# Performance work log

Hardware: AMD Instinct MI355X
Metric: run time of the kernel (lower is better)

## Reference

```python
import jax, jax.numpy as jnp
import numpy as np

B, S, HID, H = 1, 2048, 512, 8
D = HID // H            # head_dim = 64
N_TIP, N_FAC = 16, 256
SCALE = 1.0 / np.sqrt(D).astype(np.float32)


def _dominant_dim_indices():
    # dominant_fcs = arange(n_tip) % (head_dim//2), identical for every head
    pair_dim = max(1, D // 2)
    fc = jnp.arange(N_TIP) % pair_dim                      # [n_tip]
    dim_idx = jnp.stack((fc * 2, fc * 2 + 1), axis=-1).reshape(-1)  # [2*n_tip]
    return jnp.clip(dim_idx, 0, D - 1)


def setup_inputs() -> dict:
    key = jax.random.key(0)
    kx, kq, kk, kv, ko = jax.random.split(key, 5)
    s = 1.0 / np.sqrt(HID)
    return {
        "x": jax.random.normal(kx, (B, S, HID), jnp.float32),
        "wq": jax.random.normal(kq, (HID, HID), jnp.float32) * s,
        "wk": jax.random.normal(kk, (HID, HID), jnp.float32) * s,
        "wv": jax.random.normal(kv, (HID, HID), jnp.float32) * s,
        "wo": jax.random.normal(ko, (HID, HID), jnp.float32) * s,
    }


def reference(x, wq, wk, wv, wo):
    # projections (nn.Linear, no bias): y = x @ W.T; split into heads -> [B,H,S,D]
    def split_heads(y):
        return y.reshape(B, S, H, D).transpose(0, 2, 1, 3)

    q = split_heads(x @ wq.T)
    k = split_heads(x @ wk.T)
    v = split_heads(x @ wv.T)

    dim_idx = _dominant_dim_indices()                      # [2*n_tip]
    q_sub = q[..., dim_idx]                                # [B,H,S,2*n_tip]
    k_sub = k[..., dim_idx]
    importance = jnp.einsum("bhqf,bhkf->bhqk", q_sub, k_sub)  # [B,H,S,S]

    n_sel = min(N_FAC, S)
    _, top_idx = jax.lax.top_k(importance, n_sel)          # [B,H,S,n_sel]

    # gather selected K/V per query: [B,H,S,n_sel,D]
    k_sel = jnp.take_along_axis(k[:, :, None], top_idx[..., None], axis=3)
    v_sel = jnp.take_along_axis(v[:, :, None], top_idx[..., None], axis=3)

    scores = jnp.einsum("bhqd,bhqkd->bhqk", q, k_sel) * SCALE
    attn = jax.nn.softmax(scores, axis=-1)
    out = jnp.einsum("bhqk,bhqkd->bhqd", attn, v_sel)      # [B,H,S,D]

    out = out.transpose(0, 2, 1, 3).reshape(B, S, HID)
    return out @ wo.T
```

## Files before the change

kernel.cpp:

```cpp
#include <hip/hip_runtime.h>

#define S_LEN  2048
#define HIDDEN 512
#define NHEAD  8
#define DHEAD  64
#define NSEL   256
#define ROWS_A 8
#define SCALE_ 0.125f

#define WAVE_SYNC() __asm__ volatile("s_waitcnt lgkmcnt(0)" ::: "memory")

__device__ __forceinline__ unsigned mapu(float f) {
  unsigned u = __float_as_uint(f);
  return (u & 0x80000000u) ? ~u : (u | 0x80000000u);
}
__device__ __forceinline__ float unmapu(unsigned x) {
  return __uint_as_float((x & 0x80000000u) ? (x & 0x7FFFFFFFu) : ~x);
}

union H4 { _Float16 h[4]; uint2 u2; };

__device__ __forceinline__ void gemm_nt_body(const float* __restrict__ A,
                                             const float* __restrict__ B,
                                             float* __restrict__ C,
                                             int K, int N, int m0, int n0,
                                             float (*As)[68], float (*Bs)[68]) {
  const int t  = threadIdx.x;
  const int tx = t & 15, ty = t >> 4;
  const int rr = t >> 3, cc = (t & 7) << 2;
  float acc[4][4] = {};

  float4 fa0 = *(const float4*)&A[(size_t)(m0 + rr)      * K + cc];
  float4 fa1 = *(const float4*)&A[(size_t)(m0 + rr + 32) * K + cc];
  float4 fb0 = *(const float4*)&B[(size_t)(n0 + rr)      * K + cc];
  float4 fb1 = *(const float4*)&B[(size_t)(n0 + rr + 32) * K + cc];

  for (int k0 = 0; k0 < K; k0 += 32) {
    __syncthreads();
    As[cc + 0][rr] = fa0.x; As[cc + 1][rr] = fa0.y; As[cc + 2][rr] = fa0.z; As[cc + 3][rr] = fa0.w;
    As[cc + 0][rr + 32] = fa1.x; As[cc + 1][rr + 32] = fa1.y; As[cc + 2][rr + 32] = fa1.z; As[cc + 3][rr + 32] = fa1.w;
    Bs[cc + 0][rr] = fb0.x; Bs[cc + 1][rr] = fb0.y; Bs[cc + 2][rr] = fb0.z; Bs[cc + 3][rr] = fb0.w;
    Bs[cc + 0][rr + 32] = fb1.x; Bs[cc + 1][rr + 32] = fb1.y; Bs[cc + 2][rr + 32] = fb1.z; Bs[cc + 3][rr + 32] = fb1.w;
    __syncthreads();
    if (k0 + 32 < K) {
      fa0 = *(const float4*)&A[(size_t)(m0 + rr)      * K + k0 + 32 + cc];
      fa1 = *(const float4*)&A[(size_t)(m0 + rr + 32) * K + k0 + 32 + cc];
      fb0 = *(const float4*)&B[(size_t)(n0 + rr)      * K + k0 + 32 + cc];
      fb1 = *(const float4*)&B[(size_t)(n0 + rr + 32) * K + k0 + 32 + cc];
    }
#pragma unroll
    for (int kk = 0; kk < 32; ++kk) {
      const float4 a4 = *(const float4*)&As[kk][ty * 4];
      const float4 b4 = *(const float4*)&Bs[kk][tx * 4];
      const float a[4] = {a4.x, a4.y, a4.z, a4.w};
      const float b[4] = {b4.x, b4.y, b4.z, b4.w};
#pragma unroll
      for (int i = 0; i < 4; ++i)
#pragma unroll
        for (int j = 0; j < 4; ++j) acc[i][j] += a[i] * b[j];
    }
  }
#pragma unroll
  for (int i = 0; i < 4; ++i) {
    float4 o = make_float4(acc[i][0], acc[i][1], acc[i][2], acc[i][3]);
    *(float4*)&C[(size_t)(m0 + ty * 4 + i) * N + n0 + tx * 4] = o;
  }
}

__global__ __launch_bounds__(256) void gemm_nt(const float* __restrict__ A,
                                               const float* __restrict__ B,
                                               float* __restrict__ C,
                                               int M, int N, int K) {
  __shared__ float As[32][68];
  __shared__ float Bs[32][68];
  gemm_nt_body(A, B, C, K, N, blockIdx.x * 64, blockIdx.y * 64, As, Bs);
}

__global__ __launch_bounds__(256) void gemm_qkv(const float* __restrict__ x,
                                                const float* __restrict__ wq,
                                                const float* __restrict__ wk,
                                                const float* __restrict__ wv,
                                                float* __restrict__ Qb,
                                                float* __restrict__ Kb,
                                                float* __restrict__ Vb) {
  __shared__ float As[32][68];
  __shared__ float Bs[32][68];
  const int z = blockIdx.z;
  const float* B = (z == 0) ? wq : (z == 1) ? wk : wv;
  float*       C = (z == 0) ? Qb : (z == 1) ? Kb : Vb;
  gemm_nt_body(x, B, C, HIDDEN, HIDDEN, blockIdx.x * 64, blockIdx.y * 64, As, Bs);
}

__global__ __launch_bounds__(256) void score_gemm(const float* __restrict__ Q,
                                                  const float* __restrict__ K,
                                                  unsigned* __restrict__ impu,
                                                  _Float16* __restrict__ sch) {
  __shared__ float Qs[64][132];
  __shared__ float Ks[64][68];
  const int bid  = blockIdx.x;
  const int h    = bid & (NHEAD - 1);
  const int tile = bid >> 3;
  const int q0   = (tile & 15) * 128;
  const int k0   = (tile >> 4) * 64;
  const int t  = threadIdx.x;
  const int tx = t & 15, ty = t >> 4;

#pragma unroll
  for (int s = 0; s < 8; ++s) {
    const int sf = s * 256 + t;
    const int r = sf >> 4, c = (sf & 15) * 4;
    const float4 f = *(const float4*)&Q[(size_t)(q0 + r) * HIDDEN + h * DHEAD + c];
    Qs[c + 0][r] = f.x; Qs[c + 1][r] = f.y; Qs[c + 2][r] = f.z; Qs[c + 3][r] = f.w;
  }
#pragma unroll
  for (int s = 0; s < 4; ++s) {
    const int sf = s * 256 + t;
    const int r = sf >> 4, c = (sf & 15) * 4;
    const float4 f = *(const float4*)&K[(size_t)(k0 + r) * HIDDEN + h * DHEAD + c];
    Ks[c + 0][r] = f.x; Ks[c + 1][r] = f.y; Ks[c + 2][r] = f.z; Ks[c + 3][r] = f.w;
  }
  __syncthreads();

  float acc[8][4] = {};
#pragma unroll
  for (int d = 0; d < 32; ++d) {
    const float4 aa = *(const float4*)&Qs[d][ty * 8];
    const float4 ab = *(const float4*)&Qs[d][ty * 8 + 4];
    const float4 b4 = *(const float4*)&Ks[d][tx * 4];
    const float a[8] = {aa.x, aa.y, aa.z, aa.w, ab.x, ab.y, ab.z, ab.w};
    const float b[4] = {b4.x, b4.y, b4.z, b4.w};
#pragma unroll
    for (int i = 0; i < 8; ++i)
#pragma unroll
      for (int j = 0; j < 4; ++j) acc[i][j] += a[i] * b[j];
  }
  float simp[8][4];
#pragma unroll
  for (int i = 0; i < 8; ++i)
#pragma unroll
    for (int j = 0; j < 4; ++j) simp[i][j] = acc[i][j];
#pragma unroll
  for (int d = 32; d < 64; ++d) {
    const float4 aa = *(const float4*)&Qs[d][ty * 8];
    const float4 ab = *(const float4*)&Qs[d][ty * 8 + 4];
    const float4 b4 = *(const float4*)&Ks[d][tx * 4];
    const float a[8] = {aa.x, aa.y, aa.z, aa.w, ab.x, ab.y, ab.z, ab.w};
    const float b[4] = {b4.x, b4.y, b4.z, b4.w};
#pragma unroll
    for (int i = 0; i < 8; ++i)
#pragma unroll
      for (int j = 0; j < 4; ++j) acc[i][j] += a[i] * b[j];
  }

#pragma unroll
  for (int i = 0; i < 8; ++i) {
    const size_t gr = (size_t)(h * S_LEN) + q0 + ty * 8 + i;
    const size_t off = gr * S_LEN + k0 + tx * 4;
    *(uint4*)&impu[off] = make_uint4(mapu(simp[i][0]), mapu(simp[i][1]),
                                     mapu(simp[i][2]), mapu(simp[i][3]));
    H4 pk;
#pragma unroll
    for (int j = 0; j < 4; ++j) pk.h[j] = (_Float16)(acc[i][j] * SCALE_);
    *(uint2*)&sch[off] = pk.u2;
  }
}

__global__ __launch_bounds__(512) void fused_select_pv(const unsigned* __restrict__ impu,
                                                       const _Float16* __restrict__ sch,
                                                       const float* __restrict__ V,
                                                       float* __restrict__ AO) {
  __shared__ unsigned hist[ROWS_A][256];
  __shared__ float    sbuf[ROWS_A][NSEL];
  __shared__ unsigned ibuf[ROWS_A][NSEL];
  __shared__ unsigned short eqbuf[ROWS_A][64];
  __shared__ unsigned rstate[ROWS_A][2];

  const int t = threadIdx.x, wv = t >> 6, lane = t & 63;
  const unsigned long long lmask = (1ull << lane) - 1ull;
  const size_t gr = (size_t)blockIdx.x * ROWS_A + wv;
  const unsigned* rowp  = impu + gr * S_LEN;
  const _Float16* shrow = sch  + gr * S_LEN;

  uint4 u[8];
  H4    s4[8];
#pragma unroll
  for (int j = 0; j < 8; ++j) {
    u[j]     = *(const uint4*)&rowp[j * 256 + lane * 4];
    s4[j].u2 = *(const uint2*)&shrow[j * 256 + lane * 4];
  }

  unsigned um = u[0].x, uM = u[0].x;
#pragma unroll
  for (int j = 0; j < 8; ++j) {
    um = min(um, min(min(u[j].x, u[j].y), min(u[j].z, u[j].w)));
    uM = max(uM, max(max(u[j].x, u[j].y), max(u[j].z, u[j].w)));
  }
#pragma unroll
  for (int off = 32; off; off >>= 1) {
    um = min(um, (unsigned)__shfl_xor((int)um, off));
    uM = max(uM, (unsigned)__shfl_xor((int)uM, off));
  }

  unsigned bn[8];
  unsigned T;
  if (uM == um) {
    T = uM;
  } else {
    const float vmin  = unmapu(um);
    const float scale = 255.0f / (unmapu(uM) - vmin);

    *(uint4*)&hist[wv][lane * 4] = make_uint4(0u, 0u, 0u, 0u);
    WAVE_SYNC();
#pragma unroll
    for (int j = 0; j < 8; ++j) {
      const unsigned uu[4] = {u[j].x, u[j].y, u[j].z, u[j].w};
      unsigned pk = 0;
#pragma unroll
      for (int e = 0; e < 4; ++e) {
        int bb = (int)((unmapu(uu[e]) - vmin) * scale);
        bb = bb < 0 ? 0 : (bb > 255 ? 255 : bb);
        pk |= (unsigned)bb << (8 * e);
        atomicAdd(&hist[wv][bb], 1u);
      }
      bn[j] = pk;
    }
    WAVE_SYNC();
    {
      const int g = 63 - lane;
      const uint4 c4 = *(const uint4*)&hist[wv][4 * g];
      const unsigned c0 = c4.x, c1 = c4.y, c2 = c4.z, c3 = c4.w;
      const unsigned lsum = c0 + c1 + c2 + c3;
      unsigned incl = lsum;
#pragma unroll
      for (int off = 1; off < 64; off <<= 1) {
        unsigned o = __shfl_up(incl, off);
        if (lane >= off) incl += o;
      }
      const unsigned excl = incl - lsum;
      const unsigned ab3 = excl, ab2 = excl + c3, ab1 = excl + c3 + c2, ab0 = excl + c3 + c2 + c1;
      if (ab3 < NSEL && NSEL <= ab3 + c3) { rstate[wv][0] = 4u*g+3u; rstate[wv][1] = NSEL - ab3; }
      if (ab2 < NSEL && NSEL <= ab2 + c2) { rstate[wv][0] = 4u*g+2u; rstate[wv][1] = NSEL - ab2; }
      if (ab1 < NSEL && NSEL <= ab1 + c1) { rstate[wv][0] = 4u*g+1u; rstate[wv][1] = NSEL - ab1; }
      if (ab0 < NSEL && NSEL <= ab0 + c0) { rstate[wv][0] = 4u*g+0u; rstate[wv][1] = NSEL - ab0; }
    }
    WAVE_SYNC();
    const unsigned B    = rstate[wv][0];
    const unsigned krem = rstate[wv][1];
    const unsigned nb   = hist[wv][B];

    if (nb <= 64) {
      unsigned* ebufu = (unsigned*)&sbuf[wv][0];
      unsigned nbase = 0;
#pragma unroll
      for (int j = 0; j < 8; ++j) {
        const unsigned uu[4] = {u[j].x, u[j].y, u[j].z, u[j].w};
#pragma unroll
        for (int e = 0; e < 4; ++e) {
          const bool inb = (((bn[j] >> (8 * e)) & 0xFFu) == B);
          const unsigned long long m = __ballot(inb);
          if (inb) ebufu[nbase + (unsigned)__popcll(m & lmask)] = uu[e];
          nbase += (unsigned)__popcll(m);
        }
      }
      WAVE_SYNC();
      const unsigned myv = (lane < (int)nb) ? ebufu[lane] : 0u;
      unsigned gtc = 0, eqc = 0;
      for (unsigned jj = 0; jj < nb; ++jj) {
        const unsigned bv = (unsigned)__shfl((int)myv, (int)jj);
        gtc += (bv > myv) ? 1u : 0u;
        eqc += (bv == myv) ? 1u : 0u;
      }
      if (lane < (int)nb && gtc < krem && krem <= gtc + eqc) rstate[wv][0] = myv;
      WAVE_SYNC();
      T = rstate[wv][0];
    } else {
      unsigned m2min = 0xFFFFFFFFu, m2max = 0u;
      for (int i = lane; i < S_LEN; i += 64) {
        const unsigned x = rowp[i];
        int bb = (int)((unmapu(x) - vmin) * scale);
        bb = bb < 0 ? 0 : (bb > 255 ? 255 : bb);
        if (bb == (int)B) { m2min = min(m2min, x); m2max = max(m2max, x); }
      }
#pragma unroll
      for (int off = 32; off; off >>= 1) {
        m2min = min(m2min, (unsigned)__shfl_xor((int)m2min, off));
        m2max = max(m2max, (unsigned)__shfl_xor((int)m2max, off));
      }
      if (m2max == m2min) {
        T = m2max;
      } else {
        const float vlo2   = unmapu(m2min);
        const float scale2 = 255.0f / (unmapu(m2max) - vlo2);
        *(uint4*)&hist[wv][lane * 4] = make_uint4(0u, 0u, 0u, 0u);
        WAVE_SYNC();
        for (int i = lane; i < S_LEN; i += 64) {
          const unsigned x = rowp[i];
          const float v = unmapu(x);
          int bb = (int)((v - vmin) * scale);
          bb = bb < 0 ? 0 : (bb > 255 ? 255 : bb);
          if (bb == (int)B) {
            int b2 = (int)((v - vlo2) * scale2);
            b2 = b2 < 0 ? 0 : (b2 > 255 ? 255 : b2);
            atomicAdd(&hist[wv][b2], 1u);
          }
        }
        WAVE_SYNC();
        {
          const int g = 63 - lane;
          const uint4 c4 = *(const uint4*)&hist[wv][4 * g];
          const unsigned c0 = c4.x, c1 = c4.y, c2 = c4.z, c3 = c4.w;
          const unsigned lsum = c0 + c1 + c2 + c3;
          unsigned incl = lsum;
#pragma unroll
          for (int off = 1; off < 64; off <<= 1) {
            unsigned o = __shfl_up(incl, off);
            if (lane >= off) incl += o;
          }
          const unsigned excl = incl - lsum;
          const unsigned ab3 = excl, ab2 = excl + c3, ab1 = excl + c3 + c2, ab0 = excl + c3 + c2 + c1;
          if (ab3 < krem && krem <= ab3 + c3) { rstate[wv][0] = 4u*g+3u; rstate[wv][1] = krem - ab3; }
          if (ab2 < krem && krem <= ab2 + c2) { rstate[wv][0] = 4u*g+2u; rstate[wv][1] = krem - ab2; }
          if (ab1 < krem && krem <= ab1 + c1) { rstate[wv][0] = 4u*g+1u; rstate[wv][1] = krem - ab1; }
          if (ab0 < krem && krem <= ab0 + c0) { rstate[wv][0] = 4u*g+0u; rstate[wv][1] = krem - ab0; }
        }
        WAVE_SYNC();
        const unsigned B2    = rstate[wv][0];
        const unsigned krem2 = rstate[wv][1];
        const unsigned nb2   = hist[wv][B2];
        if (nb2 <= 64) {
          unsigned* ebufu = (unsigned*)&sbuf[wv][0];
          unsigned nbase = 0;
          for (int i = lane; i < S_LEN; i += 64) {
            const unsigned x = rowp[i];
            const float v = unmapu(x);
            int bb = (int)((v - vmin) * scale);
            bb = bb < 0 ? 0 : (bb > 255 ? 255 : bb);
            bool inb = false;
            if (bb == (int)B) {
              int b2 = (int)((v - vlo2) * scale2);
              b2 = b2 < 0 ? 0 : (b2 > 255 ? 255 : b2);
              inb = (b2 == (int)B2);
            }
            const unsigned long long m = __ballot(inb);
            if (inb) ebufu[nbase + (unsigned)__popcll(m & lmask)] = x;
            nbase += (unsigned)__popcll(m);
          }
          WAVE_SYNC();
          const unsigned myv = (lane < (int)nb2) ? ebufu[lane] : 0u;
          unsigned gtc = 0, eqc = 0;
          for (unsigned jj = 0; jj < nb2; ++jj) {
            const unsigned bv = (unsigned)__shfl((int)myv, (int)jj);
            gtc += (bv > myv) ? 1u : 0u;
            eqc += (bv == myv) ? 1u : 0u;
          }
          if (lane < (int)nb2 && gtc < krem2 && krem2 <= gtc + eqc) rstate[wv][0] = myv;
          WAVE_SYNC();
          T = rstate[wv][0];
        } else {
          if (lane == 0) {
            unsigned pfx = 0, kr = NSEL;
            for (int rb = 3; rb >= 0; --rb) {
              for (int i2 = 0; i2 < 256; ++i2) hist[wv][i2] = 0u;
              for (int i2 = 0; i2 < S_LEN; ++i2) {
                const unsigned x = rowp[i2];
                if (rb == 3 || ((x >> (rb * 8 + 8)) == pfx)) hist[wv][(x >> (rb * 8)) & 0xFF]++;
              }
              unsigned cum = 0, sel = 0;
              for (int bb2 = 255; bb2 >= 0; --bb2) {
                if (kr <= cum + hist[wv][bb2]) { sel = (unsigned)bb2; kr -= cum; break; }
                cum += hist[wv][bb2];
              }
              pfx = (pfx << 8) | sel;
            }
            rstate[wv][0] = pfx;
          }
          WAVE_SYNC();
          T = rstate[wv][0];
        }
      }
    }
  }

  unsigned base_gt = 0, base_eq = 0;
#pragma unroll
  for (int j = 0; j < 8; ++j) {
    const unsigned uu[4] = {u[j].x, u[j].y, u[j].z, u[j].w};
#pragma unroll
    for (int e = 0; e < 4; ++e) {
      const unsigned v = uu[e];
      const int i = j * 256 + lane * 4 + e;
      const bool gt = (v > T), eq = (v == T);
      const unsigned long long mg = __ballot(gt);
      const unsigned long long me = __ballot(eq);
      if (gt) {
        const unsigned p = base_gt + (unsigned)__popcll(mg & lmask);
        ibuf[wv][p] = (unsigned)i << 9;
        sbuf[wv][p] = (float)s4[j].h[e];
      }
      if (eq) {
        const unsigned p = base_eq + (unsigned)__popcll(me & lmask);
        if (p < 64) eqbuf[wv][p] = (unsigned short)i;
      }
      base_gt += (unsigned)__popcll(mg);
      base_eq += (unsigned)__popcll(me);
    }
  }
  WAVE_SYNC();
  const unsigned ngt = base_gt, ne = base_eq;
  const unsigned need = NSEL - ngt;
  if (ne == need && ne <= 64) {
    for (unsigned j = lane; j < ne; j += 64) {
      const unsigned short ix = eqbuf[wv][j];
      ibuf[wv][ngt + j] = (unsigned)ix << 9;
      sbuf[wv][ngt + j] = (float)shrow[ix];
    }
  } else if (lane == 0) {
    if (ne <= 64) {
      for (unsigned j = 0; j < need; ++j) {
        const unsigned short ix = eqbuf[wv][j];
        ibuf[wv][ngt + j] = (unsigned)ix << 9;
        sbuf[wv][ngt + j] = (float)shrow[ix];
      }
    } else {
      unsigned taken = 0;
      for (int i = 0; i < S_LEN && taken < need; ++i)
        if (rowp[i] == T) { ibuf[wv][ngt + taken] = (unsigned)i << 9; sbuf[wv][ngt + taken] = (float)shrow[i]; ++taken; }
    }
  }
  WAVE_SYNC();

  float sc[4];
#pragma unroll
  for (int m = 0; m < 4; ++m) sc[m] = sbuf[wv][lane * 4 + m];
  float mx = fmaxf(fmaxf(sc[0], sc[1]), fmaxf(sc[2], sc[3]));
#pragma unroll
  for (int off = 32; off; off >>= 1) mx = fmaxf(mx, __shfl_xor(mx, off));
  float zs = 0.f;
#pragma unroll
  for (int m = 0; m < 4; ++m) { sc[m] = expf(sc[m] - mx); zs += sc[m]; }
#pragma unroll
  for (int off = 32; off; off >>= 1) zs += __shfl_xor(zs, off);
  const float rz = 1.0f / zs;
  *(float4*)&sbuf[wv][lane * 4] = make_float4(sc[0], sc[1], sc[2], sc[3]);
  WAVE_SYNC();

  const int h = (int)(gr >> 11), q = (int)(gr & (S_LEN - 1));
  const float* Vhl = V + h * DHEAD + lane;
  float outv = 0.f;
#pragma unroll 8
  for (int j = 0; j < NSEL; j += 4) {
    const uint4  id4 = *(const uint4*)&ibuf[wv][j];
    const float4 w4  = *(const float4*)&sbuf[wv][j];
    outv += w4.x * Vhl[id4.x];
    outv += w4.y * Vhl[id4.y];
    outv += w4.z * Vhl[id4.z];
    outv += w4.w * Vhl[id4.w];
  }
  AO[(size_t)q * HIDDEN + h * DHEAD + lane] = outv * rz;
}

__global__ __launch_bounds__(256) void imp_gemm(const float* __restrict__ Q,
                                                const float* __restrict__ K,
                                                unsigned* __restrict__ impu) {
  __shared__ float Qs[32][68];
  __shared__ float Ks[32][68];
  const int bid  = blockIdx.x;
  const int h    = bid & (NHEAD - 1);
  const int tile = bid >> 3;
  const int q0   = (tile & 31) * 64;
  const int k0   = (tile >> 5) * 64;
  const int t  = threadIdx.x;
  const int tx = t & 15, ty = t >> 4;
#pragma unroll
  for (int s = 0; s < 2; ++s) {
    int slot = t + s * 256;
    int r = slot >> 3, c = (slot & 7) << 2;
    const float4 fq = *(const float4*)&Q[(size_t)(q0 + r) * HIDDEN + h * DHEAD + c];
    Qs[c + 0][r] = fq.x; Qs[c + 1][r] = fq.y; Qs[c + 2][r] = fq.z; Qs[c + 3][r] = fq.w;
    const float4 fk = *(const float4*)&K[(size_t)(k0 + r) * HIDDEN + h * DHEAD + c];
    Ks[c + 0][r] = fk.x; Ks[c + 1][r] = fk.y; Ks[c + 2][r] = fk.z; Ks[c + 3][r] = fk.w;
  }
  __syncthreads();
  float acc[4][4] = {};
#pragma unroll
  for (int d = 0; d < 32; ++d) {
    const float4 a4 = *(const float4*)&Qs[d][ty * 4];
    const float4 b4 = *(const float4*)&Ks[d][tx * 4];
    const float a[4] = {a4.x, a4.y, a4.z, a4.w};
    const float b[4] = {b4.x, b4.y, b4.z, b4.w};
#pragma unroll
    for (int i = 0; i < 4; ++i)
#pragma unroll
      for (int j = 0; j < 4; ++j) acc[i][j] += a[i] * b[j];
  }
#pragma unroll
  for (int i = 0; i < 4; ++i) {
    uint4 o = make_uint4(mapu(acc[i][0]), mapu(acc[i][1]), mapu(acc[i][2]), mapu(acc[i][3]));
    *(uint4*)&impu[((size_t)(h * S_LEN) + q0 + ty * 4 + i) * S_LEN + k0 + tx * 4] = o;
  }
}

__global__ __launch_bounds__(512) void radix_select(const unsigned* __restrict__ impu,
                                                    unsigned short* __restrict__ selg) {
  __shared__ unsigned hist[ROWS_A][256];
  __shared__ unsigned short selbuf[ROWS_A][NSEL];
  __shared__ unsigned short eqbuf[ROWS_A][64];
  __shared__ unsigned cnt[ROWS_A], eqcnt[ROWS_A];
  __shared__ unsigned rstate[ROWS_A][2];

  const int t = threadIdx.x, wv = t >> 6, lane = t & 63;
  const size_t gr = (size_t)blockIdx.x * ROWS_A + wv;
  const unsigned* rowp = impu + gr * S_LEN;

  uint4 u[8];
#pragma unroll
  for (int j = 0; j < 8; ++j) u[j] = *(const uint4*)&rowp[j * 256 + lane * 4];

  unsigned prefix = 0, krem = NSEL;
#pragma unroll 1
  for (int b = 3; b >= 0; --b) {
    hist[wv][lane] = 0; hist[wv][lane + 64] = 0; hist[wv][lane + 128] = 0; hist[wv][lane + 192] = 0;
    WAVE_SYNC();
    const int shift = b * 8;
#pragma unroll
    for (int j = 0; j < 8; ++j) {
      const unsigned uu[4] = {u[j].x, u[j].y, u[j].z, u[j].w};
#pragma unroll
      for (int e = 0; e < 4; ++e) {
        const unsigned v = uu[e];
        const bool ok = (b == 3) || ((v >> (shift + 8)) == prefix);
        if (ok) atomicAdd(&hist[wv][(v >> shift) & 0xFF], 1u);
      }
    }
    WAVE_SYNC();
    const int g = 63 - lane;
    const uint4 c4 = *(const uint4*)&hist[wv][4 * g];
    const unsigned c0 = c4.x, c1 = c4.y, c2 = c4.z, c3 = c4.w;
    const unsigned lsum = c0 + c1 + c2 + c3;
    unsigned incl = lsum;
#pragma unroll
    for (int off = 1; off < 64; off <<= 1) {
      unsigned o = __shfl_up(incl, off);
      if (lane >= off) incl += o;
    }
    const unsigned excl = incl - lsum;
    const unsigned ab3 = excl, ab2 = excl + c3, ab1 = excl + c3 + c2, ab0 = excl + c3 + c2 + c1;
    if (ab3 < krem && krem <= ab3 + c3) { rstate[wv][0] = 4u*g+3u; rstate[wv][1] = krem - ab3; }
    if (ab2 < krem && krem <= ab2 + c2) { rstate[wv][0] = 4u*g+2u; rstate[wv][1] = krem - ab2; }
    if (ab1 < krem && krem <= ab1 + c1) { rstate[wv][0] = 4u*g+1u; rstate[wv][1] = krem - ab1; }
    if (ab0 < krem && krem <= ab0 + c0) { rstate[wv][0] = 4u*g+0u; rstate[wv][1] = krem - ab0; }
    WAVE_SYNC();
    prefix = (prefix << 8) | rstate[wv][0];
    krem   = rstate[wv][1];
  }
  const unsigned T = prefix;

  if (lane == 0) { cnt[wv] = 0; eqcnt[wv] = 0; }
  WAVE_SYNC();
#pragma unroll
  for (int j = 0; j < 8; ++j) {
    const unsigned uu[4] = {u[j].x, u[j].y, u[j].z, u[j].w};
#pragma unroll
    for (int e = 0; e < 4; ++e) {
      const unsigned v = uu[e];
      const int i = j * 256 + lane * 4 + e;
      if (v > T)       { unsigned p = atomicAdd(&cnt[wv], 1u);   selbuf[wv][p] = (unsigned short)i; }
      else if (v == T) { unsigned p = atomicAdd(&eqcnt[wv], 1u); if (p < 64) eqbuf[wv][p] = (unsigned short)i; }
    }
  }
  WAVE_SYNC();
  const unsigned ngt = cnt[wv], ne = eqcnt[wv];
  const unsigned need = NSEL - ngt;
  if (ne == need && ne <= 64) {
    for (unsigned j = lane; j < ne; j += 64) selbuf[wv][ngt + j] = eqbuf[wv][j];
  } else if (lane == 0) {
    if (ne <= 64) {
      for (unsigned a = 1; a < ne; ++a) {
        unsigned short kv = eqbuf[wv][a]; int bp = (int)a;
        while (bp > 0 && eqbuf[wv][bp - 1] > kv) { eqbuf[wv][bp] = eqbuf[wv][bp - 1]; --bp; }
        eqbuf[wv][bp] = kv;
      }
      for (unsigned j = 0; j < need; ++j) selbuf[wv][ngt + j] = eqbuf[wv][j];
    } else {
      unsigned taken = 0;
      for (int i = 0; i < S_LEN && taken < need; ++i)
        if (rowp[i] == T) { selbuf[wv][ngt + taken] = (unsigned short)i; ++taken; }
    }
  }
  WAVE_SYNC();
  if (lane < 32) {
    const uint4 o = *(const uint4*)&selbuf[wv][lane * 8];
    *(uint4*)&selg[gr * NSEL + lane * 8] = o;
  }
}

__global__ __launch_bounds__(256, 4) void fasa_attend(const float* __restrict__ Q,
                                                      const float* __restrict__ K,
                                                      const float* __restrict__ V,
                                                      const unsigned short* __restrict__ selg,
                                                      float* __restrict__ O) {
  __shared__ float qs[4][DHEAD];
  __shared__ float wbuf[4][NSEL];
  __shared__ int   ibuf[4][NSEL];
  const int bid = blockIdx.x;
  const int h   = bid & (NHEAD - 1);
  const int qb  = bid >> 3;
  const int t   = threadIdx.x, wv = t >> 6, lane = t & 63;
  const int row = qb * 4 + wv;

  qs[wv][lane] = Q[(size_t)row * HIDDEN + h * DHEAD + lane];
  const unsigned short* srow = selg + ((size_t)(h * S_LEN) + row) * NSEL;
  const ushort4 s4 = *(const ushort4*)&srow[lane * 4];
  int sidx[4] = {(int)s4.x, (int)s4.y, (int)s4.z, (int)s4.w};
  WAVE_SYNC();

  const float* Kh = K + h * DHEAD;
  float sc[4] = {0.f, 0.f, 0.f, 0.f};
#pragma unroll
  for (int k4 = 0; k4 < 16; ++k4) {
    const float4 qv = *(const float4*)&qs[wv][k4 * 4];
#pragma unroll
    for (int m = 0; m < 4; ++m) {
      const float4 kf = *(const float4*)&Kh[(size_t)sidx[m] * HIDDEN + k4 * 4];
      sc[m] += kf.x * qv.x + kf.y * qv.y + kf.z * qv.z + kf.w * qv.w;
    }
  }
#pragma unroll
  for (int m = 0; m < 4; ++m) sc[m] *= SCALE_;

  float mx = fmaxf(fmaxf(sc[0], sc[1]), fmaxf(sc[2], sc[3]));
#pragma unroll
  for (int off = 32; off; off >>= 1) mx = fmaxf(mx, __shfl_xor(mx, off));
  float zs = 0.f;
#pragma unroll
  for (int m = 0; m < 4; ++m) { sc[m] = expf(sc[m] - mx); zs += sc[m]; }
#pragma unroll
  for (int off = 32; off; off >>= 1) zs += __shfl_xor(zs, off);
  const float rz = 1.0f / zs;

  *(float4*)&wbuf[wv][lane * 4] = make_float4(sc[0], sc[1], sc[2], sc[3]);
  *(int4*)&ibuf[wv][lane * 4]   = make_int4(sidx[0], sidx[1], sidx[2], sidx[3]);
  WAVE_SYNC();

  const float* Vh = V + h * DHEAD;
  float outv = 0.f;
#pragma unroll 4
  for (int j = 0; j < NSEL; j += 4) {
    const int4   id4 = *(const int4*)&ibuf[wv][j];
    const float4 w4  = *(const float4*)&wbuf[wv][j];
    outv += w4.x * Vh[(size_t)id4.x * HIDDEN + lane];
    outv += w4.y * Vh[(size_t)id4.y * HIDDEN + lane];
    outv += w4.z * Vh[(size_t)id4.z * HIDDEN + lane];
    outv += w4.w * Vh[(size_t)id4.w * HIDDEN + lane];
  }
  O[(size_t)row * HIDDEN + h * DHEAD + lane] = outv * rz;
}

extern "C" void kernel_launch(void* const* d_in, const int* in_sizes, int n_in,
                              void* d_out, int out_size, void* d_ws, size_t ws_size,
                              hipStream_t stream) {
  const float* x  = (const float*)d_in[0];
  const float* wq = (const float*)d_in[1];
  const float* wk = (const float*)d_in[2];
  const float* wv = (const float*)d_in[3];
  const float* wo = (const float*)d_in[4];
  float* out = (float*)d_out;

  float* Qb = (float*)d_ws;
  float* Kb = Qb + (size_t)S_LEN * HIDDEN;
  float* Vb = Kb + (size_t)S_LEN * HIDDEN;
  float* AO = Vb + (size_t)S_LEN * HIDDEN;
  void*  tail = (void*)(AO + (size_t)S_LEN * HIDDEN);

  const size_t elems = (size_t)NHEAD * S_LEN * S_LEN;
  const size_t base  = (size_t)4 * S_LEN * HIDDEN * 4;
  const size_t need_new = base + elems * 4 + elems * 2;

  dim3 g(S_LEN / 64, HIDDEN / 64);
  gemm_qkv<<<dim3(S_LEN / 64, HIDDEN / 64, 3), 256, 0, stream>>>(x, wq, wk, wv, Qb, Kb, Vb);
  if (ws_size >= need_new) {
    unsigned* impu = (unsigned*)tail;
    _Float16* sch  = (_Float16*)(impu + elems);
    score_gemm<<<dim3(NHEAD * 16 * 32), 256, 0, stream>>>(Qb, Kb, impu, sch);
    fused_select_pv<<<dim3(NHEAD * S_LEN / ROWS_A), 512, 0, stream>>>(impu, sch, Vb, AO);
  } else {
    unsigned short* selg = (unsigned short*)tail;
    unsigned* impu = (unsigned*)(selg + (size_t)NHEAD * S_LEN * NSEL);
    imp_gemm<<<dim3(NHEAD * 32 * 32), 256, 0, stream>>>(Qb, Kb, impu);
    radix_select<<<dim3(NHEAD * S_LEN / ROWS_A), 512, 0, stream>>>(impu, selg);
    fasa_attend<<<dim3((S_LEN / 4) * NHEAD), 256, 0, stream>>>(Qb, Kb, Vb, selg, AO);
  }
  gemm_nt<<<g, 256, 0, stream>>>(AO, wo, out, S_LEN, HIDDEN, HIDDEN);
}
```

Measured before the change: 224.7 us.

## Fuse score GEMM with top-k select and PV into one LDS-resident kernel

Merges the score GEMM and the select/softmax/PV kernel into a single kernel. Each 512-thread block computes the importance and score rows for 8 queries of one head directly into LDS, then runs the radix select from LDS, which removes the large global writes and reads of the full S×S importance and score matrices. The cost is low arithmetic reuse, since every block streams all of K for its head and reads Q rows straight from global memory inside the inner loop. The heavy LDS use (about 136 KB per block) also limits occupancy, and a tie-sorting step is added to the serial fallback path.

New measurement: 519.9 us. 2.31x slower.

```diff
diff --git a/kernel.cpp b/kernel.cpp
--- a/kernel.cpp
+++ b/kernel.cpp
@@ -5,7 +5,7 @@
 #define NHEAD  8
 #define DHEAD  64
 #define NSEL   256
-#define ROWS_A 8
+#define ROWS_M 8
 #define SCALE_ 0.125f
 
 #define WAVE_SYNC() __asm__ volatile("s_waitcnt lgkmcnt(0)" ::: "memory")
@@ -91,95 +91,91 @@
   gemm_nt_body(x, B, C, HIDDEN, HIDDEN, blockIdx.x * 64, blockIdx.y * 64, As, Bs);
 }
 
-__global__ __launch_bounds__(256) void score_gemm(const float* __restrict__ Q,
-                                                  const float* __restrict__ K,
-                                                  unsigned* __restrict__ impu,
-                                                  _Float16* __restrict__ sch) {
-  __shared__ float Qs[64][132];
-  __shared__ float Ks[64][68];
-  const int bid  = blockIdx.x;
-  const int h    = bid & (NHEAD - 1);
-  const int tile = bid >> 3;
-  const int q0   = (tile & 15) * 128;
-  const int k0   = (tile >> 4) * 64;
-  const int t  = threadIdx.x;
-  const int tx = t & 15, ty = t >> 4;
-
-#pragma unroll
-  for (int s = 0; s < 8; ++s) {
-    const int sf = s * 256 + t;
-    const int r = sf >> 4, c = (sf & 15) * 4;
-    const float4 f = *(const float4*)&Q[(size_t)(q0 + r) * HIDDEN + h * DHEAD + c];
-    Qs[c + 0][r] = f.x; Qs[c + 1][r] = f.y; Qs[c + 2][r] = f.z; Qs[c + 3][r] = f.w;
-  }
-#pragma unroll
-  for (int s = 0; s < 4; ++s) {
-    const int sf = s * 256 + t;
-    const int r = sf >> 4, c = (sf & 15) * 4;
-    const float4 f = *(const float4*)&K[(size_t)(k0 + r) * HIDDEN + h * DHEAD + c];
-    Ks[c + 0][r] = f.x; Ks[c + 1][r] = f.y; Ks[c + 2][r] = f.z; Ks[c + 3][r] = f.w;
+__global__ __launch_bounds__(512) void mega_attn(const float* __restrict__ Qb,
+                                                 const float* __restrict__ Kb,
+                                                 const float* __restrict__ Vb,
+                                                 float* __restrict__ AO) {
+  __shared__ unsigned impL[ROWS_M][S_LEN];
+  __shared__ _Float16 scoreL[ROWS_M][S_LEN];
+  __shared__ __align__(16) char upool[40960];
+
+  float (*Kt)[20]            = (float (*)[20])upool;
+  unsigned (*hist)[256]      = (unsigned (*)[256])upool;
+  float (*sbuf)[256]         = (float (*)[256])(upool + 8192);
+  unsigned (*ibuf)[256]      = (unsigned (*)[256])(upool + 16384);
+  unsigned short (*eqbuf)[64]= (unsigned short (*)[64])(upool + 24576);
+  unsigned (*rstate)[2]      = (unsigned (*)[2])(upool + 25600);
+
+  const int bid = blockIdx.x;
+  const int h   = bid & (NHEAD - 1);
+  const int qb  = bid >> 3;
+  const int t   = threadIdx.x;
+  const int wv  = t >> 6, lane = t & 63;
+
+  {
+    float acc[ROWS_M], simp[ROWS_M];
+#pragma unroll
+    for (int r = 0; r < ROWS_M; ++r) acc[r] = 0.f;
+
+    float4 pf[4];
+#pragma unroll
+    for (int i = 0; i < 4; ++i) {
+      const int s = t + 512 * i;
+      const int key = s >> 2, part = (s & 3) * 4;
+      pf[i] = *(const float4*)&Kb[(size_t)key * HIDDEN + h * DHEAD + part];
+    }
+
+#pragma unroll 1
+    for (int cc = 0; cc < 16; ++cc) {
+      const int ks = cc >> 2, dc = cc & 3;
+      __syncthreads();
+#pragma unroll
+      for (int i = 0; i < 4; ++i) {
+        const int s = t + 512 * i;
+        *(float4*)&Kt[s >> 2][(s & 3) * 4] = pf[i];
+      }
+      __syncthreads();
+      if (cc < 15) {
+        const int nks = (cc + 1) >> 2, ndc = (cc + 1) & 3;
+#pragma unroll
+        for (int i = 0; i < 4; ++i) {
+          const int s = t + 512 * i;
+          const int key = s >> 2, part = (s & 3) * 4;
+          pf[i] = *(const float4*)&Kb[(size_t)(nks * 512 + key) * HIDDEN + h * DHEAD + ndc * 16 + part];
+        }
+      }
+      const float4 ka = *(const float4*)&Kt[t][0];
+      const float4 kb = *(const float4*)&Kt[t][4];
+      const float4 kc = *(const float4*)&Kt[t][8];
+      const float4 kd = *(const float4*)&Kt[t][12];
+      const float kk[16] = {ka.x, ka.y, ka.z, ka.w, kb.x, kb.y, kb.z, kb.w,
+                            kc.x, kc.y, kc.z, kc.w, kd.x, kd.y, kd.z, kd.w};
+#pragma unroll
+      for (int r = 0; r < ROWS_M; ++r) {
+        const float* qp = &Qb[(size_t)(qb * ROWS_M + r) * HIDDEN + h * DHEAD + dc * 16];
+#pragma unroll
+        for (int dd = 0; dd < 16; ++dd) acc[r] += kk[dd] * qp[dd];
+      }
+      if (dc == 1) {
+#pragma unroll
+        for (int r = 0; r < ROWS_M; ++r) simp[r] = acc[r];
+      }
+      if (dc == 3) {
+#pragma unroll
+        for (int r = 0; r < ROWS_M; ++r) {
+          impL[r][ks * 512 + t]   = mapu(simp[r]);
+          scoreL[r][ks * 512 + t] = (_Float16)(acc[r] * SCALE_);
+        }
+#pragma unroll
+        for (int r = 0; r < ROWS_M; ++r) acc[r] = 0.f;
+      }
+    }
   }
   __syncthreads();
 
-  float acc[8][4] = {};
-#pragma unroll
-  for (int d = 0; d < 32; ++d) {
-    const float4 aa = *(const float4*)&Qs[d][ty * 8];
-    const float4 ab = *(const float4*)&Qs[d][ty * 8 + 4];
-    const float4 b4 = *(const float4*)&Ks[d][tx * 4];
-    const float a[8] = {aa.x, aa.y, aa.z, aa.w, ab.x, ab.y, ab.z, ab.w};
-    const float b[4] = {b4.x, b4.y, b4.z, b4.w};
-#pragma unroll
-    for (int i = 0; i < 8; ++i)
-#pragma unroll
-      for (int j = 0; j < 4; ++j) acc[i][j] += a[i] * b[j];
-  }
-  float simp[8][4];
-#pragma unroll
-  for (int i = 0; i < 8; ++i)
-#pragma unroll
-    for (int j = 0; j < 4; ++j) simp[i][j] = acc[i][j];
-#pragma unroll
-  for (int d = 32; d < 64; ++d) {
-    const float4 aa = *(const float4*)&Qs[d][ty * 8];
-    const float4 ab = *(const float4*)&Qs[d][ty * 8 + 4];
-    const float4 b4 = *(const float4*)&Ks[d][tx * 4];
-    const float a[8] = {aa.x, aa.y, aa.z, aa.w, ab.x, ab.y, ab.z, ab.w};
-    const float b[4] = {b4.x, b4.y, b4.z, b4.w};
-#pragma unroll
-    for (int i = 0; i < 8; ++i)
-#pragma unroll
-      for (int j = 0; j < 4; ++j) acc[i][j] += a[i] * b[j];
-  }
-
-#pragma unroll
-  for (int i = 0; i < 8; ++i) {
-    const size_t gr = (size_t)(h * S_LEN) + q0 + ty * 8 + i;
-    const size_t off = gr * S_LEN + k0 + tx * 4;
-    *(uint4*)&impu[off] = make_uint4(mapu(simp[i][0]), mapu(simp[i][1]),
-                                     mapu(simp[i][2]), mapu(simp[i][3]));
-    H4 pk;
-#pragma unroll
-    for (int j = 0; j < 4; ++j) pk.h[j] = (_Float16)(acc[i][j] * SCALE_);
-    *(uint2*)&sch[off] = pk.u2;
-  }
-}
-
-__global__ __launch_bounds__(512) void fused_select_pv(const unsigned* __restrict__ impu,
-                                                       const _Float16* __restrict__ sch,
-                                                       const float* __restrict__ V,
-                                                       float* __restrict__ AO) {
-  __shared__ unsigned hist[ROWS_A][256];
-  __shared__ float    sbuf[ROWS_A][NSEL];
-  __shared__ unsigned ibuf[ROWS_A][NSEL];
-  __shared__ unsigned short eqbuf[ROWS_A][64];
-  __shared__ unsigned rstate[ROWS_A][2];
-
-  const int t = threadIdx.x, wv = t >> 6, lane = t & 63;
   const unsigned long long lmask = (1ull << lane) - 1ull;
-  const size_t gr = (size_t)blockIdx.x * ROWS_A + wv;
-  const unsigned* rowp  = impu + gr * S_LEN;
-  const _Float16* shrow = sch  + gr * S_LEN;
+  const unsigned* rowp  = &impL[wv][0];
+  const _Float16* shrow = &scoreL[wv][0];
 
   uint4 u[8];
   H4    s4[8];
@@ -416,6 +412,11 @@
     }
   } else if (lane == 0) {
     if (ne <= 64) {
+      for (unsigned a = 1; a < ne; ++a) {
+        unsigned short kv = eqbuf[wv][a]; int bp = (int)a;
+        while (bp > 0 && eqbuf[wv][bp - 1] > kv) { eqbuf[wv][bp] = eqbuf[wv][bp - 1]; --bp; }
+        eqbuf[wv][bp] = kv;
+      }
       for (unsigned j = 0; j < need; ++j) {
         const unsigned short ix = eqbuf[wv][j];
         ibuf[wv][ngt + j] = (unsigned)ix << 9;
@@ -444,8 +445,8 @@
   *(float4*)&sbuf[wv][lane * 4] = make_float4(sc[0], sc[1], sc[2], sc[3]);
   WAVE_SYNC();
 
-  const int h = (int)(gr >> 11), q = (int)(gr & (S_LEN - 1));
-  const float* Vhl = V + h * DHEAD + lane;
+  const int q = qb * ROWS_M + wv;
+  const float* Vhl = Vb + h * DHEAD + lane;
   float outv = 0.f;
 #pragma unroll 8
   for (int j = 0; j < NSEL; j += 4) {
@@ -459,203 +460,6 @@
   AO[(size_t)q * HIDDEN + h * DHEAD + lane] = outv * rz;
 }
 
-__global__ __launch_bounds__(256) void imp_gemm(const float* __restrict__ Q,
-                                                const float* __restrict__ K,
-                                                unsigned* __restrict__ impu) {
-  __shared__ float Qs[32][68];
-  __shared__ float Ks[32][68];
-  const int bid  = blockIdx.x;
-  const int h    = bid & (NHEAD - 1);
-  const int tile = bid >> 3;
-  const int q0   = (tile & 31) * 64;
-  const int k0   = (tile >> 5) * 64;
-  const int t  = threadIdx.x;
-  const int tx = t & 15, ty = t >> 4;
-#pragma unroll
-  for (int s = 0; s < 2; ++s) {
-    int slot = t + s * 256;
-    int r = slot >> 3, c = (slot & 7) << 2;
-    const float4 fq = *(const float4*)&Q[(size_t)(q0 + r) * HIDDEN + h * DHEAD + c];
-    Qs[c + 0][r] = fq.x; Qs[c + 1][r] = fq.y; Qs[c + 2][r] = fq.z; Qs[c + 3][r] = fq.w;
-    const float4 fk = *(const float4*)&K[(size_t)(k0 + r) * HIDDEN + h * DHEAD + c];
-    Ks[c + 0][r] = fk.x; Ks[c + 1][r] = fk.y; Ks[c + 2][r] = fk.z; Ks[c + 3][r] = fk.w;
-  }
-  __syncthreads();
-  float acc[4][4] = {};
-#pragma unroll
-  for (int d = 0; d < 32; ++d) {
-    const float4 a4 = *(const float4*)&Qs[d][ty * 4];
-    const float4 b4 = *(const float4*)&Ks[d][tx * 4];
-    const float a[4] = {a4.x, a4.y, a4.z, a4.w};
-    const float b[4] = {b4.x, b4.y, b4.z, b4.w};
-#pragma unroll
-    for (int i = 0; i < 4; ++i)
-#pragma unroll
-      for (int j = 0; j < 4; ++j) acc[i][j] += a[i] * b[j];
-  }
-#pragma unroll
-  for (int i = 0; i < 4; ++i) {
-    uint4 o = make_uint4(mapu(acc[i][0]), mapu(acc[i][1]), mapu(acc[i][2]), mapu(acc[i][3]));
-    *(uint4*)&impu[((size_t)(h * S_LEN) + q0 + ty * 4 + i) * S_LEN + k0 + tx * 4] = o;
-  }
-}
-
-__global__ __launch_bounds__(512) void radix_select(const unsigned* __restrict__ impu,
-                                                    unsigned short* __restrict__ selg) {
-  __shared__ unsigned hist[ROWS_A][256];
-  __shared__ unsigned short selbuf[ROWS_A][NSEL];
-  __shared__ unsigned short eqbuf[ROWS_A][64];
-  __shared__ unsigned cnt[ROWS_A], eqcnt[ROWS_A];
-  __shared__ unsigned rstate[ROWS_A][2];
-
-  const int t = threadIdx.x, wv = t >> 6, lane = t & 63;
-  const size_t gr = (size_t)blockIdx.x * ROWS_A + wv;
-  const unsigned* rowp = impu + gr * S_LEN;
-
-  uint4 u[8];
-#pragma unroll
-  for (int j = 0; j < 8; ++j) u[j] = *(const uint4*)&rowp[j * 256 + lane * 4];
-
-  unsigned prefix = 0, krem = NSEL;
-#pragma unroll 1
-  for (int b = 3; b >= 0; --b) {
-    hist[wv][lane] = 0; hist[wv][lane + 64] = 0; hist[wv][lane + 128] = 0; hist[wv][lane + 192] = 0;
-    WAVE_SYNC();
-    const int shift = b * 8;
-#pragma unroll
-    for (int j = 0; j < 8; ++j) {
-      const unsigned uu[4] = {u[j].x, u[j].y, u[j].z, u[j].w};
-#pragma unroll
-      for (int e = 0; e < 4; ++e) {
-        const unsigned v = uu[e];
-        const bool ok = (b == 3) || ((v >> (shift + 8)) == prefix);
-        if (ok) atomicAdd(&hist[wv][(v >> shift) & 0xFF], 1u);
-      }
-    }
-    WAVE_SYNC();
-    const int g = 63 - lane;
-    const uint4 c4 = *(const uint4*)&hist[wv][4 * g];
-    const unsigned c0 = c4.x, c1 = c4.y, c2 = c4.z, c3 = c4.w;
-    const unsigned lsum = c0 + c1 + c2 + c3;
-    unsigned incl = lsum;
-#pragma unroll
-    for (int off = 1; off < 64; off <<= 1) {
-      unsigned o = __shfl_up(incl, off);
-      if (lane >= off) incl += o;
-    }
-    const unsigned excl = incl - lsum;
-    const unsigned ab3 = excl, ab2 = excl + c3, ab1 = excl + c3 + c2, ab0 = excl + c3 + c2 + c1;
-    if (ab3 < krem && krem <= ab3 + c3) { rstate[wv][0] = 4u*g+3u; rstate[wv][1] = krem - ab3; }
-    if (ab2 < krem && krem <= ab2 + c2) { rstate[wv][0] = 4u*g+2u; rstate[wv][1] = krem - ab2; }
-    if (ab1 < krem && krem <= ab1 + c1) { rstate[wv][0] = 4u*g+1u; rstate[wv][1] = krem - ab1; }
-    if (ab0 < krem && krem <= ab0 + c0) { rstate[wv][0] = 4u*g+0u; rstate[wv][1] = krem - ab0; }
-    WAVE_SYNC();
-    prefix = (prefix << 8) | rstate[wv][0];
-    krem   = rstate[wv][1];
-  }
-  const unsigned T = prefix;
-
-  if (lane == 0) { cnt[wv] = 0; eqcnt[wv] = 0; }
-  WAVE_SYNC();
-#pragma unroll
-  for (int j = 0; j < 8; ++j) {
-    const unsigned uu[4] = {u[j].x, u[j].y, u[j].z, u[j].w};
-#pragma unroll
-    for (int e = 0; e < 4; ++e) {
-      const unsigned v = uu[e];
-      const int i = j * 256 + lane * 4 + e;
-      if (v > T)       { unsigned p = atomicAdd(&cnt[wv], 1u);   selbuf[wv][p] = (unsigned short)i; }
-      else if (v == T) { unsigned p = atomicAdd(&eqcnt[wv], 1u); if (p < 64) eqbuf[wv][p] = (unsigned short)i; }
-    }
-  }
-  WAVE_SYNC();
-  const unsigned ngt = cnt[wv], ne = eqcnt[wv];
-  const unsigned need = NSEL - ngt;
-  if (ne == need && ne <= 64) {
-    for (unsigned j = lane; j < ne; j += 64) selbuf[wv][ngt + j] = eqbuf[wv][j];
-  } else if (lane == 0) {
-    if (ne <= 64) {
-      for (unsigned a = 1; a < ne; ++a) {
-        unsigned short kv = eqbuf[wv][a]; int bp = (int)a;
-        while (bp > 0 && eqbuf[wv][bp - 1] > kv) { eqbuf[wv][bp] = eqbuf[wv][bp - 1]; --bp; }
-        eqbuf[wv][bp] = kv;
-      }
-      for (unsigned j = 0; j < need; ++j) selbuf[wv][ngt + j] = eqbuf[wv][j];
-    } else {
-      unsigned taken = 0;
-      for (int i = 0; i < S_LEN && taken < need; ++i)
-        if (rowp[i] == T) { selbuf[wv][ngt + taken] = (unsigned short)i; ++taken; }
-    }
-  }
-  WAVE_SYNC();
-  if (lane < 32) {
-    const uint4 o = *(const uint4*)&selbuf[wv][lane * 8];
-    *(uint4*)&selg[gr * NSEL + lane * 8] = o;
-  }
-}
-
-__global__ __launch_bounds__(256, 4) void fasa_attend(const float* __restrict__ Q,
-                                                      const float* __restrict__ K,
-                                                      const float* __restrict__ V,
-                                                      const unsigned short* __restrict__ selg,
-                                                      float* __restrict__ O) {
-  __shared__ float qs[4][DHEAD];
-  __shared__ float wbuf[4][NSEL];
-  __shared__ int   ibuf[4][NSEL];
-  const int bid = blockIdx.x;
-  const int h   = bid & (NHEAD - 1);
-  const int qb  = bid >> 3;
-  const int t   = threadIdx.x, wv = t >> 6, lane = t & 63;
-  const int row = qb * 4 + wv;
-
-  qs[wv][lane] = Q[(size_t)row * HIDDEN + h * DHEAD + lane];
-  const unsigned short* srow = selg + ((size_t)(h * S_LEN) + row) * NSEL;
-  const ushort4 s4 = *(const ushort4*)&srow[lane * 4];
-  int sidx[4] = {(int)s4.x, (int)s4.y, (int)s4.z, (int)s4.w};
-  WAVE_SYNC();
-
-  const float* Kh = K + h * DHEAD;
-  float sc[4] = {0.f, 0.f, 0.f, 0.f};
-#pragma unroll
-  for (int k4 = 0; k4 < 16; ++k4) {
-    const float4 qv = *(const float4*)&qs[wv][k4 * 4];
-#pragma unroll
-    for (int m = 0; m < 4; ++m) {
-      const float4 kf = *(const float4*)&Kh[(size_t)sidx[m] * HIDDEN + k4 * 4];
-      sc[m] += kf.x * qv.x + kf.y * qv.y + kf.z * qv.z + kf.w * qv.w;
-    }
-  }
-#pragma unroll
-  for (int m = 0; m < 4; ++m) sc[m] *= SCALE_;
-
-  float mx = fmaxf(fmaxf(sc[0], sc[1]), fmaxf(sc[2], sc[3]));
-#pragma unroll
-  for (int off = 32; off; off >>= 1) mx = fmaxf(mx, __shfl_xor(mx, off));
-  float zs = 0.f;
-#pragma unroll
-  for (int m = 0; m < 4; ++m) { sc[m] = expf(sc[m] - mx); zs += sc[m]; }
-#pragma unroll
-  for (int off = 32; off; off >>= 1) zs += __shfl_xor(zs, off);
-  const float rz = 1.0f / zs;
-
-  *(float4*)&wbuf[wv][lane * 4] = make_float4(sc[0], sc[1], sc[2], sc[3]);
-  *(int4*)&ibuf[wv][lane * 4]   = make_int4(sidx[0], sidx[1], sidx[2], sidx[3]);
-  WAVE_SYNC();
-
-  const float* Vh = V + h * DHEAD;
-  float outv = 0.f;
-#pragma unroll 4
-  for (int j = 0; j < NSEL; j += 4) {
-    const int4   id4 = *(const int4*)&ibuf[wv][j];
-    const float4 w4  = *(const float4*)&wbuf[wv][j];
-    outv += w4.x * Vh[(size_t)id4.x * HIDDEN + lane];
-    outv += w4.y * Vh[(size_t)id4.y * HIDDEN + lane];
-    outv += w4.z * Vh[(size_t)id4.z * HIDDEN + lane];
-    outv += w4.w * Vh[(size_t)id4.w * HIDDEN + lane];
-  }
-  O[(size_t)row * HIDDEN + h * DHEAD + lane] = outv * rz;
-}
-
 extern "C" void kernel_launch(void* const* d_in, const int* in_sizes, int n_in,
                               void* d_out, int out_size, void* d_ws, size_t ws_size,
                               hipStream_t stream) {
@@ -670,25 +474,9 @@
   float* Kb = Qb + (size_t)S_LEN * HIDDEN;
   float* Vb = Kb + (size_t)S_LEN * HIDDEN;
   float* AO = Vb + (size_t)S_LEN * HIDDEN;
-  void*  tail = (void*)(AO + (size_t)S_LEN * HIDDEN);
-
-  const size_t elems = (size_t)NHEAD * S_LEN * S_LEN;
-  const size_t base  = (size_t)4 * S_LEN * HIDDEN * 4;
-  const size_t need_new = base + elems * 4 + elems * 2;
 
   dim3 g(S_LEN / 64, HIDDEN / 64);
   gemm_qkv<<<dim3(S_LEN / 64, HIDDEN / 64, 3), 256, 0, stream>>>(x, wq, wk, wv, Qb, Kb, Vb);
-  if (ws_size >= need_new) {
-    unsigned* impu = (unsigned*)tail;
-    _Float16* sch  = (_Float16*)(impu + elems);
-    score_gemm<<<dim3(NHEAD * 16 * 32), 256, 0, stream>>>(Qb, Kb, impu, sch);
-    fused_select_pv<<<dim3(NHEAD * S_LEN / ROWS_A), 512, 0, stream>>>(impu, sch, Vb, AO);
-  } else {
-    unsigned short* selg = (unsigned short*)tail;
-    unsigned* impu = (unsigned*)(selg + (size_t)NHEAD * S_LEN * NSEL);
-    imp_gemm<<<dim3(NHEAD * 32 * 32), 256, 0, stream>>>(Qb, Kb, impu);
-    radix_select<<<dim3(NHEAD * S_LEN / ROWS_A), 512, 0, stream>>>(impu, selg);
-    fasa_attend<<<dim3((S_LEN / 4) * NHEAD), 256, 0, stream>>>(Qb, Kb, Vb, selg, AO);
-  }
+  mega_attn<<<dim3(NHEAD * (S_LEN / ROWS_M)), 512, 0, stream>>>(Qb, Kb, Vb, AO);
   gemm_nt<<<g, 256, 0, stream>>>(AO, wo, out, S_LEN, HIDDEN, HIDDEN);
 }
```
